# Kernel optimization log

Hardware: AMD Instinct MI355X
Metric: run time of the kernel (lower is better)

Reference implementation:

```python
import jax, jax.numpy as jnp
import numpy as np
from jax import lax

ITER = 10
SMOOTH = 1.0


def _max_pool3(x):
    # 3x3 max pool, stride 1, pad 1 (torch pads with -inf for max pool)
    return lax.reduce_window(x, -np.inf, lax.max,
                             window_dimensions=(1, 1, 3, 3),
                             window_strides=(1, 1, 1, 1),
                             padding=((0, 0), (0, 0), (1, 1), (1, 1)))


def soft_skeletonize(x, thresh_width=ITER):
    def body(i, x):
        min_pool_x = -_max_pool3(-x)
        contour = jax.nn.relu(_max_pool3(min_pool_x) - min_pool_x)
        return jax.nn.relu(x - contour)
    return lax.fori_loop(0, thresh_width, body, x)


def setup_inputs() -> dict:
    key = jax.random.key(0)
    k1, k2 = jax.random.split(key)
    shape = (32, 2, 512, 512)
    y_pred = jax.random.uniform(k1, shape, dtype=jnp.float32)
    y_true = jax.random.uniform(k2, shape, dtype=jnp.float32)
    return {"y_pred": y_pred, "y_true": y_true}


def reference(y_pred, y_true):
    skel_pred = soft_skeletonize(y_pred, ITER)
    skel_true = soft_skeletonize(y_true, ITER)
    tprec = (jnp.sum((skel_pred * y_true)[:, 1:]) + SMOOTH) / (jnp.sum(skel_pred[:, 1:]) + SMOOTH)
    tsens = (jnp.sum((skel_true * y_pred)[:, 1:]) + SMOOTH) / (jnp.sum(skel_true[:, 1:]) + SMOOTH)
    cl_dice = 1.0 - 2.0 * (tprec * tsens) / (tprec + tsens)
    return cl_dice
```

## Files before the change

### kernel.cpp

```cpp
#include <hip/hip_runtime.h>

#define IMG 512
#define HW (IMG * IMG)
#define NB 32
#define NIMG 64
#define BAND 16
#define NBAND (IMG / BAND)
#define NSTG 5
#define HALO (2 * NSTG)
#define NSTEP ((BAND + 2 * HALO) / 2)
#define INF __builtin_inff()

static __device__ __forceinline__ float dpp_from_prev(float v, float ident) {
    return __int_as_float(__builtin_amdgcn_update_dpp(
        __float_as_int(ident), __float_as_int(v), 0x138, 0xF, 0xF, false));
}
static __device__ __forceinline__ float dpp_from_next(float v, float ident) {
    return __int_as_float(__builtin_amdgcn_update_dpp(
        __float_as_int(ident), __float_as_int(v), 0x130, 0xF, 0xF, false));
}

struct Row { float4 a, b; };

static __device__ __forceinline__ float min3f(float a, float b, float c) { return fminf(fminf(a, b), c); }
static __device__ __forceinline__ float max3f(float a, float b, float c) { return fmaxf(fmaxf(a, b), c); }

static __device__ __forceinline__ Row splat(float v) {
    Row r;
    r.a = make_float4(v, v, v, v);
    r.b = make_float4(v, v, v, v);
    return r;
}

static __device__ __forceinline__ Row rmin3(const Row& x, const Row& y, const Row& z) {
    Row o;
    const float* px = (const float*)&x;
    const float* py = (const float*)&y;
    const float* pz = (const float*)&z;
    float* po = (float*)&o;
#pragma unroll
    for (int i = 0; i < 8; ++i) po[i] = min3f(px[i], py[i], pz[i]);
    return o;
}

static __device__ __forceinline__ Row rmax3(const Row& x, const Row& y, const Row& z) {
    Row o;
    const float* px = (const float*)&x;
    const float* py = (const float*)&y;
    const float* pz = (const float*)&z;
    float* po = (float*)&o;
#pragma unroll
    for (int i = 0; i < 8; ++i) po[i] = max3f(px[i], py[i], pz[i]);
    return o;
}

static __device__ __forceinline__ Row hmin3(const Row& v) {
    float shl = dpp_from_prev(v.b.w, INF);
    float shr = dpp_from_next(v.a.x, INF);
    Row o;
    o.a.x = min3f(shl,   v.a.x, v.a.y);
    o.a.y = min3f(v.a.x, v.a.y, v.a.z);
    o.a.z = min3f(v.a.y, v.a.z, v.a.w);
    o.a.w = min3f(v.a.z, v.a.w, v.b.x);
    o.b.x = min3f(v.a.w, v.b.x, v.b.y);
    o.b.y = min3f(v.b.x, v.b.y, v.b.z);
    o.b.z = min3f(v.b.y, v.b.z, v.b.w);
    o.b.w = min3f(v.b.z, v.b.w, shr);
    return o;
}

static __device__ __forceinline__ Row hmax3(const Row& v) {
    float shl = dpp_from_prev(v.b.w, -INF);
    float shr = dpp_from_next(v.a.x, -INF);
    Row o;
    o.a.x = max3f(shl,   v.a.x, v.a.y);
    o.a.y = max3f(v.a.x, v.a.y, v.a.z);
    o.a.z = max3f(v.a.y, v.a.z, v.a.w);
    o.a.w = max3f(v.a.z, v.a.w, v.b.x);
    o.b.x = max3f(v.a.w, v.b.x, v.b.y);
    o.b.y = max3f(v.b.x, v.b.y, v.b.z);
    o.b.z = max3f(v.b.y, v.b.z, v.b.w);
    o.b.w = max3f(v.b.z, v.b.w, shr);
    return o;
}

template <bool EDGE>
static __device__ __forceinline__ void step2(Row (&x)[2], Row (&mn)[2],
                                             Row& in0, Row& in1, int t) {
    Row vmin0 = rmin3(x[0], x[1], in0);
    Row vmin1 = rmin3(x[1], in0, in1);
    Row mna = hmin3(vmin0);
    Row mnb = hmin3(vmin1);
    if (EDGE) {
        if ((unsigned)(t - 1) >= IMG) mna = splat(-INF);
        if ((unsigned)t >= IMG) mnb = splat(-INF);
    }
    Row vmax0 = rmax3(mn[0], mn[1], mna);
    Row vmax1 = rmax3(mn[1], mna, mnb);
    Row mp0 = hmax3(vmax0);
    Row mp1 = hmax3(vmax1);
    Row out0, out1;
    {
        const float* px0 = (const float*)&x[0];
        const float* px1 = (const float*)&x[1];
        const float* pm1 = (const float*)&mn[1];
        const float* pma = (const float*)&mna;
        const float* pp0 = (const float*)&mp0;
        const float* pp1 = (const float*)&mp1;
        float* po0 = (float*)&out0;
        float* po1 = (float*)&out1;
#pragma unroll
        for (int i = 0; i < 8; ++i) {
            po0[i] = fmaxf(px0[i] - fmaxf(pp0[i] - pm1[i], 0.f), 0.f);
            po1[i] = fmaxf(px1[i] - fmaxf(pp1[i] - pma[i], 0.f), 0.f);
        }
    }
    if (EDGE) {
        if ((unsigned)(t - 2) >= IMG) out0 = splat(INF);
        if ((unsigned)(t - 1) >= IMG) out1 = splat(INF);
    }
    x[0] = in0;  x[1] = in1;
    mn[0] = mna; mn[1] = mnb;
    in0 = out0;  in1 = out1;
}

static __device__ __forceinline__ Row load_or_inf(const float* __restrict__ p, int r, int lane) {
    if ((unsigned)r >= IMG) return splat(INF);
    const float4* q = (const float4*)(p + (size_t)r * IMG + lane * 8);
    Row o;
    o.a = q[0];
    o.b = q[1];
    return o;
}

template <bool EDGE>
static __device__ __forceinline__ void run_a(const float* __restrict__ src,
                                             float* __restrict__ dst, int B, int lane) {
    Row x[NSTG][2], mn[NSTG][2];
#pragma unroll
    for (int j = 0; j < NSTG; ++j) {
        x[j][0] = splat(INF);   x[j][1] = splat(INF);
        mn[j][0] = splat(-INF); mn[j][1] = splat(-INF);
    }
    Row pre0 = load_or_inf(src, B - HALO, lane);
    Row pre1 = load_or_inf(src, B - HALO + 1, lane);
#pragma unroll 1
    for (int k = 0; k < NSTEP; ++k) {
        const int t = B - HALO + 2 * k;
        Row in0 = pre0, in1 = pre1;
        const int tp = (k + 1 < NSTEP) ? t + 2 : -1;
        pre0 = load_or_inf(src, tp, lane);
        pre1 = load_or_inf(src, tp + 1, lane);
#pragma unroll
        for (int j = 0; j < NSTG; ++j)
            step2<EDGE>(x[j], mn[j], in0, in1, t - 2 * j);
        const int v = t - HALO;
        if ((unsigned)(v - B) < BAND) {
            float4* q0 = (float4*)(dst + (size_t)v * IMG + lane * 8);
            q0[0] = in0.a; q0[1] = in0.b;
            float4* q1 = (float4*)(dst + (size_t)(v + 1) * IMG + lane * 8);
            q1[0] = in1.a; q1[1] = in1.b;
        }
    }
}

__global__ __launch_bounds__(64, 2) void skel5_a(const float* __restrict__ yp,
                                                 const float* __restrict__ yt,
                                                 float* __restrict__ mid) {
    const int blk = blockIdx.x;
    const int img = blk >> 5, band = blk & (NBAND - 1);
    const float* src = (img < NB) ? yp + (size_t)(2 * img + 1) * HW
                                  : yt + (size_t)(2 * (img - NB) + 1) * HW;
    float* dst = mid + (size_t)img * HW;
    const int lane = threadIdx.x;
    const int B = band * BAND;
    if (band == 0 || band == NBAND - 1) run_a<true>(src, dst, B, lane);
    else                                run_a<false>(src, dst, B, lane);
}

template <bool EDGE>
static __device__ __forceinline__ void run_b(const float* __restrict__ src,
                                             const float* __restrict__ wp, int B, int lane,
                                             float& s_prod, float& s_val) {
    Row x[NSTG][2], mn[NSTG][2];
#pragma unroll
    for (int j = 0; j < NSTG; ++j) {
        x[j][0] = splat(INF);   x[j][1] = splat(INF);
        mn[j][0] = splat(-INF); mn[j][1] = splat(-INF);
    }
    Row pre0 = load_or_inf(src, B - HALO, lane);
    Row pre1 = load_or_inf(src, B - HALO + 1, lane);
#pragma unroll 1
    for (int k = 0; k < NSTEP; ++k) {
        const int t = B - HALO + 2 * k;
        Row in0 = pre0, in1 = pre1;
        const int tp = (k + 1 < NSTEP) ? t + 2 : -1;
        pre0 = load_or_inf(src, tp, lane);
        pre1 = load_or_inf(src, tp + 1, lane);
        const int v = t - HALO;
        const bool inband = (unsigned)(v - B) < BAND;
        Row w0, w1;
        if (inband) {
            const float4* q0 = (const float4*)(wp + (size_t)v * IMG + lane * 8);
            w0.a = q0[0]; w0.b = q0[1];
            const float4* q1 = (const float4*)(wp + (size_t)(v + 1) * IMG + lane * 8);
            w1.a = q1[0]; w1.b = q1[1];
        }
#pragma unroll
        for (int j = 0; j < NSTG; ++j)
            step2<EDGE>(x[j], mn[j], in0, in1, t - 2 * j);
        if (inband) {
            const float* p0 = (const float*)&in0;
            const float* p1 = (const float*)&in1;
            const float* q0 = (const float*)&w0;
            const float* q1 = (const float*)&w1;
#pragma unroll
            for (int i = 0; i < 8; ++i) {
                s_prod += p0[i] * q0[i] + p1[i] * q1[i];
                s_val += p0[i] + p1[i];
            }
        }
    }
}

__global__ __launch_bounds__(64, 2) void skel5_b(const float* __restrict__ mid,
                                                 const float* __restrict__ yp,
                                                 const float* __restrict__ yt,
                                                 double* __restrict__ acc) {
    const int blk = blockIdx.x;
    const int img = blk >> 5, band = blk & (NBAND - 1);
    const float* src = mid + (size_t)img * HW;
    const float* wp = (img < NB) ? yt + (size_t)(2 * img + 1) * HW
                                 : yp + (size_t)(2 * (img - NB) + 1) * HW;
    const int lane = threadIdx.x;
    const int B = band * BAND;

    float s_prod = 0.f, s_val = 0.f;
    if (band == 0 || band == NBAND - 1) run_b<true>(src, wp, B, lane, s_prod, s_val);
    else                                run_b<false>(src, wp, B, lane, s_prod, s_val);

#pragma unroll
    for (int off = 32; off; off >>= 1) {
        s_prod += __shfl_down(s_prod, off);
        s_val += __shfl_down(s_val, off);
    }
    if (lane == 0) {
        const int base = (img < NB) ? 0 : 2;
        atomicAdd(&acc[base], (double)s_prod);
        atomicAdd(&acc[base + 1], (double)s_val);
    }
}

__global__ void finalize(const double* __restrict__ acc, float* __restrict__ out) {
    double tprec = (acc[0] + 1.0) / (acc[1] + 1.0);
    double tsens = (acc[2] + 1.0) / (acc[3] + 1.0);
    out[0] = (float)(1.0 - 2.0 * (tprec * tsens) / (tprec + tsens));
}

extern "C" void kernel_launch(void* const* d_in, const int* in_sizes, int n_in,
                              void* d_out, int out_size, void* d_ws, size_t ws_size,
                              hipStream_t stream) {
    (void)in_sizes; (void)n_in; (void)out_size; (void)ws_size;
    const float* yp = (const float*)d_in[0];
    const float* yt = (const float*)d_in[1];
    float* out = (float*)d_out;

    float* mid = (float*)d_ws;
    double* acc = (double*)(mid + (size_t)NIMG * HW);

    hipMemsetAsync(acc, 0, 4 * sizeof(double), stream);

    const int grid = NIMG * NBAND;
    skel5_a<<<grid, 64, 0, stream>>>(yp, yt, mid);
    skel5_b<<<grid, 64, 0, stream>>>(mid, yp, yt, acc);
    finalize<<<1, 1, 0, stream>>>(acc, out);
}
```

Before: 259.6 us.

## Fuse finalize and memset into skeleton kernels, prefetch weights, unroll step loop

Removes the memset and finalize launches: the first kernel zeroes the accumulators and a counter, and the last block of the second kernel computes the final loss through a ticket counter. It drops a redundant relu on the contour, since the max-pool of the min-pool is always at least the min-pool. It also prefetches the weight rows one step ahead in the second kernel and unrolls the row-pair loop by two. Together these cut launch overhead and hide load latency, at the cost of more registers and an atomic ticket per block.

```diff
diff --git a/kernel.cpp b/kernel.cpp
--- a/kernel.cpp
+++ b/kernel.cpp
@@ -6,6 +6,7 @@
 #define NIMG 64
 #define BAND 16
 #define NBAND (IMG / BAND)
+#define GRID (NIMG * NBAND)
 #define NSTG 5
 #define HALO (2 * NSTG)
 #define NSTEP ((BAND + 2 * HALO) / 2)
@@ -111,8 +112,8 @@
         float* po1 = (float*)&out1;
 #pragma unroll
         for (int i = 0; i < 8; ++i) {
-            po0[i] = fmaxf(px0[i] - fmaxf(pp0[i] - pm1[i], 0.f), 0.f);
-            po1[i] = fmaxf(px1[i] - fmaxf(pp1[i] - pma[i], 0.f), 0.f);
+            po0[i] = fmaxf(px0[i] - (pp0[i] - pm1[i]), 0.f);
+            po1[i] = fmaxf(px1[i] - (pp1[i] - pma[i]), 0.f);
         }
     }
     if (EDGE) {
@@ -144,11 +145,11 @@
     }
     Row pre0 = load_or_inf(src, B - HALO, lane);
     Row pre1 = load_or_inf(src, B - HALO + 1, lane);
-#pragma unroll 1
+#pragma unroll 2
     for (int k = 0; k < NSTEP; ++k) {
         const int t = B - HALO + 2 * k;
         Row in0 = pre0, in1 = pre1;
-        const int tp = (k + 1 < NSTEP) ? t + 2 : -1;
+        const int tp = (k + 1 < NSTEP) ? t + 2 : -2;
         pre0 = load_or_inf(src, tp, lane);
         pre1 = load_or_inf(src, tp + 1, lane);
 #pragma unroll
@@ -166,8 +167,14 @@
 
 __global__ __launch_bounds__(64, 2) void skel5_a(const float* __restrict__ yp,
                                                  const float* __restrict__ yt,
-                                                 float* __restrict__ mid) {
+                                                 float* __restrict__ mid,
+                                                 double* __restrict__ acc,
+                                                 unsigned* __restrict__ counter) {
     const int blk = blockIdx.x;
+    if (blk == 0 && threadIdx.x == 0) {
+        acc[0] = 0.0; acc[1] = 0.0; acc[2] = 0.0; acc[3] = 0.0;
+        *counter = 0u;
+    }
     const int img = blk >> 5, band = blk & (NBAND - 1);
     const float* src = (img < NB) ? yp + (size_t)(2 * img + 1) * HW
                                   : yt + (size_t)(2 * (img - NB) + 1) * HW;
@@ -190,26 +197,26 @@
     }
     Row pre0 = load_or_inf(src, B - HALO, lane);
     Row pre1 = load_or_inf(src, B - HALO + 1, lane);
-#pragma unroll 1
+    Row wb0 = splat(0.f), wb1 = splat(0.f);
+#pragma unroll 2
     for (int k = 0; k < NSTEP; ++k) {
         const int t = B - HALO + 2 * k;
+        const int v = t - HALO;
         Row in0 = pre0, in1 = pre1;
-        const int tp = (k + 1 < NSTEP) ? t + 2 : -1;
+        const int tp = (k + 1 < NSTEP) ? t + 2 : -2;
         pre0 = load_or_inf(src, tp, lane);
         pre1 = load_or_inf(src, tp + 1, lane);
-        const int v = t - HALO;
-        const bool inband = (unsigned)(v - B) < BAND;
-        Row w0, w1;
-        if (inband) {
-            const float4* q0 = (const float4*)(wp + (size_t)v * IMG + lane * 8);
-            w0.a = q0[0]; w0.b = q0[1];
-            const float4* q1 = (const float4*)(wp + (size_t)(v + 1) * IMG + lane * 8);
-            w1.a = q1[0]; w1.b = q1[1];
+        const Row w0 = wb0, w1 = wb1;
+        if ((unsigned)(v + 2 - B) < BAND) {
+            const float4* q0 = (const float4*)(wp + (size_t)(v + 2) * IMG + lane * 8);
+            wb0.a = q0[0]; wb0.b = q0[1];
+            const float4* q1 = (const float4*)(wp + (size_t)(v + 3) * IMG + lane * 8);
+            wb1.a = q1[0]; wb1.b = q1[1];
         }
 #pragma unroll
         for (int j = 0; j < NSTG; ++j)
             step2<EDGE>(x[j], mn[j], in0, in1, t - 2 * j);
-        if (inband) {
+        if ((unsigned)(v - B) < BAND) {
             const float* p0 = (const float*)&in0;
             const float* p1 = (const float*)&in1;
             const float* q0 = (const float*)&w0;
@@ -226,7 +233,9 @@
 __global__ __launch_bounds__(64, 2) void skel5_b(const float* __restrict__ mid,
                                                  const float* __restrict__ yp,
                                                  const float* __restrict__ yt,
-                                                 double* __restrict__ acc) {
+                                                 double* __restrict__ acc,
+                                                 unsigned* __restrict__ counter,
+                                                 float* __restrict__ out) {
     const int blk = blockIdx.x;
     const int img = blk >> 5, band = blk & (NBAND - 1);
     const float* src = mid + (size_t)img * HW;
@@ -248,13 +257,18 @@
         const int base = (img < NB) ? 0 : 2;
         atomicAdd(&acc[base], (double)s_prod);
         atomicAdd(&acc[base + 1], (double)s_val);
-    }
-}
-
-__global__ void finalize(const double* __restrict__ acc, float* __restrict__ out) {
-    double tprec = (acc[0] + 1.0) / (acc[1] + 1.0);
-    double tsens = (acc[2] + 1.0) / (acc[3] + 1.0);
-    out[0] = (float)(1.0 - 2.0 * (tprec * tsens) / (tprec + tsens));
+        __threadfence();
+        unsigned ticket = atomicAdd(counter, 1u);
+        if (ticket == GRID - 1) {
+            double a0 = atomicAdd(&acc[0], 0.0);
+            double a1 = atomicAdd(&acc[1], 0.0);
+            double a2 = atomicAdd(&acc[2], 0.0);
+            double a3 = atomicAdd(&acc[3], 0.0);
+            double tprec = (a0 + 1.0) / (a1 + 1.0);
+            double tsens = (a2 + 1.0) / (a3 + 1.0);
+            out[0] = (float)(1.0 - 2.0 * (tprec * tsens) / (tprec + tsens));
+        }
+    }
 }
 
 extern "C" void kernel_launch(void* const* d_in, const int* in_sizes, int n_in,
@@ -267,11 +281,8 @@
 
     float* mid = (float*)d_ws;
     double* acc = (double*)(mid + (size_t)NIMG * HW);
-
-    hipMemsetAsync(acc, 0, 4 * sizeof(double), stream);
-
-    const int grid = NIMG * NBAND;
-    skel5_a<<<grid, 64, 0, stream>>>(yp, yt, mid);
-    skel5_b<<<grid, 64, 0, stream>>>(mid, yp, yt, acc);
-    finalize<<<1, 1, 0, stream>>>(acc, out);
-}
+    unsigned* counter = (unsigned*)(acc + 4);
+
+    skel5_a<<<GRID, 64, 0, stream>>>(yp, yt, mid, acc, counter);
+    skel5_b<<<GRID, 64, 0, stream>>>(mid, yp, yt, acc, counter, out);
+}
```

Result: slower. 415.6 us (+60.1%).
